# Kernel tuning notes

Hardware: AMD Instinct MI355X
Metric: run time of the kernel (lower is better)

## Reference

```python
import jax, jax.numpy as jnp
import numpy as np

# Static config (matches init_kwargs)
VOCAB, EMBED, HIDDEN = 32000, 256, 512
SLOTS, MEM_DIM, HEADS, TOPK = 1024, 64, 4, 8
B, T = 16, 128
# beta_read/beta_write are learned scalars but the torch forward detaches them
# via .item(); treat as constants (|beta| + 1e-6 with beta init ~1.0).
BETA_R = 1.0 + 1e-6
BETA_W = 1.0 + 1e-6
EPS = 1e-8


def setup_inputs() -> dict:
    key = jax.random.key(0)
    ks = jax.random.split(key, 16)
    s = 0.02
    HD = HEADS * MEM_DIM
    return {
        "input_seq": jax.random.randint(ks[0], (B, T), 0, VOCAB),
        "E": jax.random.normal(ks[1], (VOCAB, EMBED), jnp.float32) * s,
        "W_ih": jax.random.normal(ks[2], (4 * HIDDEN, EMBED + MEM_DIM), jnp.float32) * s,
        "W_hh": jax.random.normal(ks[3], (4 * HIDDEN, HIDDEN), jnp.float32) * s,
        "b_ih": jnp.zeros((4 * HIDDEN,), jnp.float32),
        "b_hh": jnp.zeros((4 * HIDDEN,), jnp.float32),
        "W_out": jax.random.normal(ks[4], (HIDDEN, VOCAB), jnp.float32) * s,
        "b_out": jnp.zeros((VOCAB,), jnp.float32),
        "W_rk": jax.random.normal(ks[5], (HIDDEN, HD), jnp.float32) * s,
        "b_rk": jnp.zeros((HD,), jnp.float32),
        "W_wk": jax.random.normal(ks[6], (HIDDEN, HD), jnp.float32) * s,
        "b_wk": jnp.zeros((HD,), jnp.float32),
        "W_wv": jax.random.normal(ks[7], (HIDDEN, HD), jnp.float32) * s,
        "b_wv": jnp.zeros((HD,), jnp.float32),
        "W_er": jax.random.normal(ks[8], (HIDDEN, HD), jnp.float32) * s,
        "b_er": jnp.zeros((HD,), jnp.float32),
    }


def _address(memory, keys, beta):
    # memory: [B,S,D], keys: [B,H,D] -> sparse (top-k) content weights [B,H,S]
    mem_n = memory / (jnp.linalg.norm(memory, axis=-1, keepdims=True) + EPS)
    key_n = keys / (jnp.linalg.norm(keys, axis=-1, keepdims=True) + EPS)
    scores = beta * jnp.einsum("bhd,bsd->bhs", key_n, mem_n)
    vals, idx = jax.lax.top_k(scores, TOPK)           # [B,H,K]
    sm = jax.nn.softmax(vals, axis=-1)                # softmax over top-k only
    w = jnp.zeros_like(scores)
    b_ix = jnp.arange(scores.shape[0])[:, None, None]
    h_ix = jnp.arange(HEADS)[None, :, None]
    return w.at[b_ix, h_ix, idx].set(sm)              # [B,H,S]


def reference(input_seq, E, W_ih, W_hh, b_ih, b_hh, W_out, b_out,
              W_rk, b_rk, W_wk, b_wk, W_wv, b_wv, W_er, b_er):
    Bq = input_seq.shape[0]
    memory0 = jnp.full((Bq, SLOTS, MEM_DIM), 1e-6, jnp.float32)
    h0 = jnp.zeros((Bq, HIDDEN), jnp.float32)
    c0 = jnp.zeros((Bq, HIDDEN), jnp.float32)
    r0 = jnp.zeros((Bq, MEM_DIM), jnp.float32)

    def step(carry, x_t):
        memory, h, c, read_vec = carry
        emb = E[x_t]                                          # [B,embed]
        inp = jnp.concatenate([emb, read_vec], axis=-1)
        gates = inp @ W_ih.T + b_ih + h @ W_hh.T + b_hh       # [B,4H]
        i, f, g, o = jnp.split(gates, 4, axis=-1)             # torch LSTM order
        c = jax.nn.sigmoid(f) * c + jax.nn.sigmoid(i) * jnp.tanh(g)
        h = jax.nn.sigmoid(o) * jnp.tanh(c)
        logits = h @ W_out + b_out                            # [B,V]
        rk = (h @ W_rk + b_rk).reshape(Bq, HEADS, MEM_DIM)
        wk = (h @ W_wk + b_wk).reshape(Bq, HEADS, MEM_DIM)
        wv = (h @ W_wv + b_wv).reshape(Bq, HEADS, MEM_DIM)
        er = jax.nn.sigmoid(h @ W_er + b_er).reshape(Bq, HEADS, MEM_DIM)
        # content-addressed top-k read
        rw = _address(memory, rk, BETA_R)                     # [B,H,S]
        read_vec = jnp.einsum("bhs,bsd->bhd", rw, memory).mean(axis=1)
        # erase + add write
        ww = _address(memory, wk, BETA_W)                     # [B,H,S]
        keep = jnp.prod(1.0 - ww[..., None] * er[:, :, None, :], axis=1)
        add = jnp.einsum("bhs,bhd->bsd", ww, wv)
        memory = memory * keep + add
        return (memory, h, c, read_vec), logits

    _, logits_seq = jax.lax.scan(step, (memory0, h0, c0, r0), input_seq.T)
    return jnp.transpose(logits_seq, (1, 0, 2))               # [B,T,V]
```

## Files before the change

kernel.cpp:

```cpp
#include <hip/hip_runtime.h>
#include <hip/hip_bf16.h>
#include <stdint.h>

typedef unsigned int uint;
typedef unsigned long long u64;

#define T_STEPS 128
#define BQ 16
#define HID 512
#define XROW 580
#define WROW 516
#define NSLOT 1024
#define MD 64
#define VOCAB 32000
#define NWG 128
#define BETA 1.000001f
#define EPSN 1e-8f

#define OFF_NRM 8704
#define OFF_WS  8832
#define OFF_SCR 12960
#define SMEM_F  22496

#define AL4(dst, p) asm volatile("global_load_dwordx4 %0, %1, off sc0 sc1" : "=v"(dst) : "v"(p))
#define ALF(dst, p) asm volatile("global_load_dword %0, %1, off sc0 sc1" : "=v"(dst) : "v"(p))
#define AWAIT() do { asm volatile("s_waitcnt vmcnt(0)" ::: "memory"); __builtin_amdgcn_sched_barrier(0); } while(0)

__device__ __forceinline__ float sigm(float x){ return 1.f/(1.f+expf(-x)); }
__device__ __forceinline__ void astoref(float* p, float v){
  __hip_atomic_store(p, v, __ATOMIC_RELAXED, __HIP_MEMORY_SCOPE_AGENT);
}
__device__ __forceinline__ void astoreu64(u64* p, u64 v){
  __hip_atomic_store(p, v, __ATOMIC_RELAXED, __HIP_MEMORY_SCOPE_AGENT);
}
__device__ __forceinline__ u64 aloadu64(const u64* p){
  return __hip_atomic_load((u64*)p, __ATOMIC_RELAXED, __HIP_MEMORY_SCOPE_AGENT);
}

__device__ __forceinline__ u64 packsc(float v, int slot){
  uint u = __float_as_uint(v);
  u = (u & 0x80000000u) ? ~u : (u | 0x80000000u);
  return ((u64)u << 10) | (u64)(1023 - slot);
}
__device__ __forceinline__ float unpackval(u64 p){
  uint u = (uint)(p >> 10);
  uint bits = (u & 0x80000000u) ? (u & 0x7fffffffu) : ~u;
  return __uint_as_float(bits);
}
__device__ __forceinline__ int unpackslot(u64 p){ return 1023 - (int)(p & 1023u); }

__device__ __forceinline__ void gbar(uint* arrv, uint& ls){
  asm volatile("s_waitcnt vmcnt(0)" ::: "memory");
  __syncthreads();
  ls++;
  if (threadIdx.x == 0)
    __hip_atomic_store(arrv + (size_t)blockIdx.x*32, ls, __ATOMIC_RELAXED, __HIP_MEMORY_SCOPE_AGENT);
  if (threadIdx.x < NWG){
    while (__hip_atomic_load(arrv + (size_t)threadIdx.x*32, __ATOMIC_RELAXED, __HIP_MEMORY_SCOPE_AGENT) < ls)
      __builtin_amdgcn_s_sleep(1);
  }
  __syncthreads();
}

__global__ __launch_bounds__(256) void prep_emb(const float* __restrict__ E,
                                                const int* __restrict__ seq,
                                                float* __restrict__ EMB){
  int m = blockIdx.x;
  int t = m >> 4, b = m & 15;
  int x = seq[b*T_STEPS + t];
  EMB[(size_t)m*256 + threadIdx.x] = E[(size_t)x*256 + threadIdx.x];
}

__global__ __launch_bounds__(256) void gemm_emb(const float* __restrict__ A,
                                                const float* __restrict__ W_ih,
                                                const float* __restrict__ b_ih,
                                                const float* __restrict__ b_hh,
                                                float* __restrict__ C){
  __shared__ __align__(16) float As[16*68];
  __shared__ __align__(16) float Bs[16*68];
  int mt = blockIdx.x & 31, nt = blockIdx.x >> 5;
  int m0 = mt*64, n0 = nt*64;
  int tx = threadIdx.x & 15, ty = threadIdx.x >> 4;
  float acc[4][4] = {};
  for (int k0 = 0; k0 < 256; k0 += 16){
    int mm = threadIdx.x >> 2, kq = (threadIdx.x & 3)*4;
    float4 a = *(const float4*)(A + (size_t)(m0+mm)*256 + k0 + kq);
    As[(kq+0)*68+mm]=a.x; As[(kq+1)*68+mm]=a.y; As[(kq+2)*68+mm]=a.z; As[(kq+3)*68+mm]=a.w;
    int pp = n0 + mm;
    int r = (pp & 3)*512 + (pp >> 2);
    float4 bv = *(const float4*)(W_ih + (size_t)r*320 + k0 + kq);
    Bs[(kq+0)*68+mm]=bv.x; Bs[(kq+1)*68+mm]=bv.y; Bs[(kq+2)*68+mm]=bv.z; Bs[(kq+3)*68+mm]=bv.w;
    __syncthreads();
    #pragma unroll
    for (int kk = 0; kk < 16; ++kk){
      float4 av = *(const float4*)(As + kk*68 + ty*4);
      float4 bb = *(const float4*)(Bs + kk*68 + tx*4);
      float aa[4] = {av.x,av.y,av.z,av.w};
      float bv2[4] = {bb.x,bb.y,bb.z,bb.w};
      #pragma unroll
      for (int i = 0; i < 4; ++i)
        #pragma unroll
        for (int j = 0; j < 4; ++j)
          acc[i][j] = fmaf(aa[i], bv2[j], acc[i][j]);
    }
    __syncthreads();
  }
  #pragma unroll
  for (int i = 0; i < 4; ++i){
    int m = m0 + ty*4 + i;
    #pragma unroll
    for (int j = 0; j < 4; ++j){
      int pp = n0 + tx*4 + j;
      int r = (pp & 3)*512 + (pp >> 2);
      C[(size_t)m*2048 + pp] = acc[i][j] + b_ih[r] + b_hh[r];
    }
  }
}

__global__ __launch_bounds__(256, 1) void recurrent_kernel(
    const float* __restrict__ W_hh, const float* __restrict__ W_ih,
    const float* __restrict__ W_rk, const float* __restrict__ b_rk,
    const float* __restrict__ W_wk, const float* __restrict__ b_wk,
    const float* __restrict__ W_wv, const float* __restrict__ b_wv,
    const float* __restrict__ W_er, const float* __restrict__ b_er,
    const float* __restrict__ G_emb, float* __restrict__ H_all,
    float* __restrict__ mem_g, float* __restrict__ projbuf,
    float* __restrict__ rv_g, u64* __restrict__ cand,
    u64* __restrict__ wlist, uint* __restrict__ arrv)
{
  __shared__ __align__(16) float smem[SMEM_F];
  const int tid = threadIdx.x;
  const int wg  = blockIdx.x;
  uint ls = 0;
  float c_reg = 0.f;

  const int p1_b = tid >> 4, p1_col = tid & 15;
  const int pcol = wg*16 + p1_col;
  const int rrow = (pcol & 3)*512 + (pcol >> 2);

  const int msel = wg >> 5;
  const int col0 = (wg & 31)*8;
  const float* Wm = (msel==0)? W_rk : (msel==1)? W_wk : (msel==2)? W_wv : W_er;
  const float* bm = (msel==0)? b_rk : (msel==1)? b_wk : (msel==2)? b_wv : b_er;
  {
    float* Ws = smem + OFF_WS;
    for (int i = tid; i < 8*HID; i += 256){
      int k = i >> 3, j = i & 7;
      Ws[j*WROW + k] = Wm[(size_t)k*256 + col0 + j];
    }
  }
  const int bb3 = wg >> 3, rg = wg & 7, s0 = rg*128;
  float* mslice_g = mem_g + ((size_t)bb3*NSLOT + s0)*MD;

  #pragma clang loop unroll(disable)
  for (int t = 0; t < T_STEPS; ++t){
    {
      float* xs = smem + OFF_SCR;
      float* gl = smem + OFF_SCR + 9280;
      if (t > 0){
        const float4* hsrc = (const float4*)(H_all + (size_t)(t-1)*BQ*HID);
        for (int i = tid; i < BQ*HID/4; i += 256){
          int b = i >> 7, q = i & 127;
          *(float4*)(xs + b*XROW + q*4) = hsrc[i];
        }
        {
          int b = tid >> 4, dq = tid & 15;
          float4 rvv;
          AL4(rvv, (const float4*)(rv_g + (size_t)b*MD) + dq);
          AWAIT();
          *(float4*)(xs + b*XROW + 512 + dq*4) = rvv;
        }
      } else {
        for (int i = tid; i < BQ*XROW; i += 256) xs[i] = 0.f;
      }
      __syncthreads();
      {
        float a0 = G_emb[(size_t)(t*BQ + p1_b)*2048 + pcol];
        float a1 = 0.f, a2 = 0.f, a3 = 0.f;
        const float4* wh = (const float4*)(W_hh + (size_t)rrow*HID);
        const float4* xv = (const float4*)(xs + p1_b*XROW);
        #pragma unroll 2
        for (int k = 0; k < 128; k += 4){
          float4 w, x;
          w=wh[k+0]; x=xv[k+0]; a0=fmaf(w.x,x.x,a0); a0=fmaf(w.y,x.y,a0); a0=fmaf(w.z,x.z,a0); a0=fmaf(w.w,x.w,a0);
          w=wh[k+1]; x=xv[k+1]; a1=fmaf(w.x,x.x,a1); a1=fmaf(w.y,x.y,a1); a1=fmaf(w.z,x.z,a1); a1=fmaf(w.w,x.w,a1);
          w=wh[k+2]; x=xv[k+2]; a2=fmaf(w.x,x.x,a2); a2=fmaf(w.y,x.y,a2); a2=fmaf(w.z,x.z,a2); a2=fmaf(w.w,x.w,a2);
          w=wh[k+3]; x=xv[k+3]; a3=fmaf(w.x,x.x,a3); a3=fmaf(w.y,x.y,a3); a3=fmaf(w.z,x.z,a3); a3=fmaf(w.w,x.w,a3);
        }
        const float4* wi = (const float4*)(W_ih + (size_t)rrow*320 + 256);
        const float4* xr = (const float4*)(xs + p1_b*XROW + 512);
        #pragma unroll
        for (int k = 0; k < 16; k += 4){
          float4 w, x;
          w=wi[k+0]; x=xr[k+0]; a0=fmaf(w.x,x.x,a0); a0=fmaf(w.y,x.y,a0); a0=fmaf(w.z,x.z,a0); a0=fmaf(w.w,x.w,a0);
          w=wi[k+1]; x=xr[k+1]; a1=fmaf(w.x,x.x,a1); a1=fmaf(w.y,x.y,a1); a1=fmaf(w.z,x.z,a1); a1=fmaf(w.w,x.w,a1);
          w=wi[k+2]; x=xr[k+2]; a2=fmaf(w.x,x.x,a2); a2=fmaf(w.y,x.y,a2); a2=fmaf(w.z,x.z,a2); a2=fmaf(w.w,x.w,a2);
          w=wi[k+3]; x=xr[k+3]; a3=fmaf(w.x,x.x,a3); a3=fmaf(w.y,x.y,a3); a3=fmaf(w.z,x.z,a3); a3=fmaf(w.w,x.w,a3);
        }
        gl[p1_b*16 + p1_col] = (a0+a1)+(a2+a3);
      }
      __syncthreads();
      if (p1_col < 4){
        float gi = gl[p1_b*16 + p1_col*4 + 0];
        float gf = gl[p1_b*16 + p1_col*4 + 1];
        float gg = gl[p1_b*16 + p1_col*4 + 2];
        float go = gl[p1_b*16 + p1_col*4 + 3];
        c_reg = sigm(gf)*c_reg + sigm(gi)*tanhf(gg);
        float h = sigm(go)*tanhf(c_reg);
        astoref(H_all + (size_t)(t*BQ + p1_b)*HID + wg*4 + p1_col, h);
      }
    }
    gbar(arrv, ls);

    {
      float* hs = smem + OFF_SCR;
      float* Ws = smem + OFF_WS;
      const float4* hsrc = (const float4*)(H_all + (size_t)t*BQ*HID);
      for (int i = tid; i < BQ*HID/4; i += 256){
        int b = i >> 7, q = i & 127;
        *(float4*)(hs + b*WROW + q*4) = hsrc[i];
      }
      __syncthreads();
      int b = tid >> 4, o2 = (tid & 15) >> 1, half = tid & 1;
      const float4* wp = (const float4*)(Ws + o2*WROW + half*256);
      const float4* xp = (const float4*)(hs + b*WROW + half*256);
      float a0 = 0.f, a1 = 0.f;
      #pragma unroll 4
      for (int k = 0; k < 64; k += 2){
        float4 w = wp[k], x = xp[k];
        a0=fmaf(w.x,x.x,a0); a0=fmaf(w.y,x.y,a0); a0=fmaf(w.z,x.z,a0); a0=fmaf(w.w,x.w,a0);
        w = wp[k+1]; x = xp[k+1];
        a1=fmaf(w.x,x.x,a1); a1=fmaf(w.y,x.y,a1); a1=fmaf(w.z,x.z,a1); a1=fmaf(w.w,x.w,a1);
      }
      float acc = a0 + a1;
      float other = __shfl_xor(acc, 1);
      if (half == 0){
        float v = acc + other + bm[col0 + o2];
        if (msel == 3) v = sigm(v);
        astoref(projbuf + (size_t)(t&1)*BQ*1024 + (size_t)b*1024 + msel*256 + col0 + o2, v);
      }
    }
    gbar(arrv, ls);

    {
      float* mem_s  = smem;
      float* nrm_s  = smem + OFF_NRM;
      float* scr    = smem + OFF_SCR;
      u64*   wl_s   = (u64*)scr;
      float* key_s  = scr + 64;
      float* er_s   = scr + 576;
      float* wv_s   = scr + 832;
      float* knrm_s = scr + 1088;
      float* sc_s   = scr + 1096;
      const int par = t & 1, parp = par ^ 1;
      const float* projb = projbuf + (size_t)par*BQ*1024 + (size_t)bb3*1024;
      const float* projp = projbuf + (size_t)parp*BQ*1024 + (size_t)bb3*1024;

      if (tid >= 128){
        int i = tid - 128;
        float4 kv;
        AL4(kv, (const float4*)projb + i);
        AWAIT();
        *(float4*)(key_s + i*4) = kv;
      } else if (t == 0){
        for (int i = tid; i < 128*MD; i += 128){
          int row = i >> 6, d = i & 63;
          mem_s[row*68 + d] = 1e-6f;
          astoref(mslice_g + i, 1e-6f);
        }
      } else {
        if (tid < 32)
          wl_s[tid] = aloadu64(wlist + (size_t)bb3*32 + tid);
        if (tid < 64){
          float4 v; AL4(v, (const float4*)(projp + 512) + tid); AWAIT();
          *(float4*)(wv_s + tid*4) = v;
        } else {
          int i = tid - 64;
          float4 v; AL4(v, (const float4*)(projp + 768) + i); AWAIT();
          *(float4*)(er_s + i*4) = v;
        }
      }
      __syncthreads();
      if (t > 0 && tid < 64){
        const int d = tid;
        #pragma unroll 1
        for (int e = 0; e < 32; ++e){
          u64 w64 = wl_s[e];
          int sl = (int)(w64 & 0xffffffffu);
          if (sl >= s0 && sl < s0+128){
            float w = __uint_as_float((uint)(w64 >> 32));
            int h = e >> 3;
            mem_s[(sl-s0)*68 + d] *= (1.f - w*er_s[h*64 + d]);
          }
        }
        #pragma unroll 1
        for (int e = 0; e < 32; ++e){
          u64 w64 = wl_s[e];
          int sl = (int)(w64 & 0xffffffffu);
          if (sl >= s0 && sl < s0+128){
            float w = __uint_as_float((uint)(w64 >> 32));
            int h = e >> 3;
            mem_s[(sl-s0)*68 + d] += w*wv_s[h*64 + d];
          }
        }
        #pragma unroll 1
        for (int e = 0; e < 32; ++e){
          u64 w64 = wl_s[e];
          int sl = (int)(w64 & 0xffffffffu);
          if (sl >= s0 && sl < s0+128)
            astoref(mslice_g + (sl-s0)*MD + d, mem_s[(sl-s0)*68 + d]);
        }
      }
      __syncthreads();
      {
        int s = tid >> 1, half = tid & 1;
        const float4* mp = (const float4*)(mem_s + s*68 + half*32);
        float sum = 0.f;
        #pragma unroll
        for (int q = 0; q < 8; ++q){
          float4 v = mp[q];
          sum = fmaf(v.x,v.x,sum); sum = fmaf(v.y,v.y,sum);
          sum = fmaf(v.z,v.z,sum); sum = fmaf(v.w,v.w,sum);
        }
        sum += __shfl_xor(sum, 1);
        if (half == 0) nrm_s[s] = sqrtf(sum) + EPSN;
      }
      if (tid < 8){
        const float4* kp = (const float4*)(key_s + tid*MD);
        float sum = 0.f;
        #pragma unroll
        for (int q = 0; q < 16; ++q){
          float4 v = kp[q];
          sum = fmaf(v.x,v.x,sum); sum = fmaf(v.y,v.y,sum);
          sum = fmaf(v.z,v.z,sum); sum = fmaf(v.w,v.w,sum);
        }
        knrm_s[tid] = sqrtf(sum) + EPSN;
      }
      __syncthreads();
      {
        int s = tid >> 1, kh = tid & 1;
        const float4* mp = (const float4*)(mem_s + s*68);
        float rnm = 1.f / nrm_s[s];
        float acc4[4] = {0.f,0.f,0.f,0.f};
        #pragma unroll
        for (int q = 0; q < 16; ++q){
          float4 m = mp[q];
          #pragma unroll
          for (int kk = 0; kk < 4; ++kk){
            float4 k4 = *(const float4*)(key_s + (kh*4+kk)*MD + q*4);
            acc4[kk] = fmaf(m.x,k4.x,acc4[kk]); acc4[kk] = fmaf(m.y,k4.y,acc4[kk]);
            acc4[kk] = fmaf(m.z,k4.z,acc4[kk]); acc4[kk] = fmaf(m.w,k4.w,acc4[kk]);
          }
        }
        #pragma unroll
        for (int kk = 0; kk < 4; ++kk){
          int key = kh*4 + kk;
          sc_s[key*128 + s] = BETA * acc4[kk] * rnm / knrm_s[key];
        }
      }
      __syncthreads();
      {
        int wid = tid >> 6, lane = tid & 63;
        #pragma unroll
        for (int kk = 0; kk < 2; ++kk){
          int key = wid*2 + kk;
          u64 p0 = packsc(sc_s[key*128 + lane],      s0 + lane);
          u64 p1 = packsc(sc_s[key*128 + 64 + lane], s0 + 64 + lane);
          #pragma unroll
          for (int r = 0; r < 8; ++r){
            u64 m = p0 > p1 ? p0 : p1;
            #pragma unroll
            for (int o = 32; o; o >>= 1){ u64 q = __shfl_xor(m, o); if (q > m) m = q; }
            if (p0 == m) p0 = 0; else if (p1 == m) p1 = 0;
            if (lane == 0) astoreu64(cand + (((size_t)bb3*8 + key)*8 + rg)*8 + r, m);
          }
        }
      }
    }
    gbar(arrv, ls);

    if (wg < BQ){
      const int bb = wg;
      float* rvp = smem + OFF_SCR;
      int wid = tid >> 6, lane = tid & 63;
      #pragma unroll
      for (int kk = 0; kk < 2; ++kk){
        int key = wid*2 + kk;
        u64 pv = aloadu64(cand + (((size_t)bb*8 + key)*8 + (lane >> 3))*8 + (lane & 7));
        u64 sel = 0;
        #pragma unroll
        for (int r = 0; r < 8; ++r){
          u64 m = pv;
          #pragma unroll
          for (int o = 32; o; o >>= 1){ u64 q = __shfl_xor(m, o); if (q > m) m = q; }
          if (pv == m) pv = 0;
          if (lane == r) sel = m;
        }
        float val = unpackval(sel);
        int slot = unpackslot(sel);
        float vmax = __shfl(val, 0);
        float e = (lane < 8) ? expf(val - vmax) : 0.f;
        float ssum = e;
        #pragma unroll
        for (int o = 32; o; o >>= 1) ssum += __shfl_xor(ssum, o);
        float w = e / ssum;
        if (key < 4){
          int sls[8];
          #pragma unroll
          for (int i = 0; i < 8; ++i) sls[i] = __shfl(slot, i);
          float mv[8];
          #pragma unroll
          for (int i = 0; i < 8; ++i)
            ALF(mv[i], mem_g + ((size_t)bb*NSLOT + sls[i])*MD + lane);
          AWAIT();
          float acc = 0.f;
          #pragma unroll
          for (int i = 0; i < 8; ++i) acc = fmaf(__shfl(w, i), mv[i], acc);
          rvp[key*64 + lane] = acc;
        } else if (lane < 8){
          astoreu64(wlist + (size_t)bb*32 + (key-4)*8 + lane,
                    ((u64)__float_as_uint(w) << 32) | (u64)(uint)slot);
        }
      }
      __syncthreads();
      if (tid < 64){
        float m = 0.25f*(rvp[tid] + rvp[64+tid] + rvp[128+tid] + rvp[192+tid]);
        astoref(rv_g + (size_t)bb*MD + tid, m);
      }
    }
    gbar(arrv, ls);
  }
}

__global__ __launch_bounds__(256) void gemm_out(const float* __restrict__ A,
                                                const float* __restrict__ Bmat,
                                                const float* __restrict__ bias,
                                                float* __restrict__ C){
  __shared__ __align__(16) float As[16*132];
  __shared__ __align__(16) float Bs[16*64];
  int mt = blockIdx.x & 15, nt = blockIdx.x >> 4;
  int m0 = mt*128, n0 = nt*64;
  int tx = threadIdx.x & 15, ty = threadIdx.x >> 4;
  float acc[8][4] = {};
  for (int k0 = 0; k0 < 512; k0 += 16){
    int mm = threadIdx.x >> 1, kq = (threadIdx.x & 1)*8;
    float4 a0 = *(const float4*)(A + (size_t)(m0+mm)*512 + k0 + kq);
    float4 a1 = *(const float4*)(A + (size_t)(m0+mm)*512 + k0 + kq + 4);
    As[(kq+0)*132+mm]=a0.x; As[(kq+1)*132+mm]=a0.y; As[(kq+2)*132+mm]=a0.z; As[(kq+3)*132+mm]=a0.w;
    As[(kq+4)*132+mm]=a1.x; As[(kq+5)*132+mm]=a1.y; As[(kq+6)*132+mm]=a1.z; As[(kq+7)*132+mm]=a1.w;
    int kk2 = threadIdx.x >> 4, nq = (threadIdx.x & 15)*4;
    *(float4*)(Bs + kk2*64 + nq) = *(const float4*)(Bmat + (size_t)(k0+kk2)*VOCAB + n0 + nq);
    __syncthreads();
    #pragma unroll
    for (int kk = 0; kk < 16; ++kk){
      float4 x0 = *(const float4*)(As + kk*132 + ty*8);
      float4 x1 = *(const float4*)(As + kk*132 + ty*8 + 4);
      float4 bv = *(const float4*)(Bs + kk*64 + tx*4);
      float aa[8] = {x0.x,x0.y,x0.z,x0.w,x1.x,x1.y,x1.z,x1.w};
      float bb[4] = {bv.x,bv.y,bv.z,bv.w};
      #pragma unroll
      for (int i = 0; i < 8; ++i)
        #pragma unroll
        for (int j = 0; j < 4; ++j)
          acc[i][j] = fmaf(aa[i], bb[j], acc[i][j]);
    }
    __syncthreads();
  }
  #pragma unroll
  for (int i = 0; i < 8; ++i){
    int m = m0 + ty*8 + i;
    int bq = m & 15, tt = m >> 4;
    float* crow = C + ((size_t)bq*T_STEPS + tt)*VOCAB + n0 + tx*4;
    #pragma unroll
    for (int j = 0; j < 4; ++j) crow[j] = acc[i][j] + bias[n0 + tx*4 + j];
  }
}

extern "C" void kernel_launch(void* const* d_in, const int* in_sizes, int n_in,
                              void* d_out, int out_size, void* d_ws, size_t ws_size,
                              hipStream_t stream){
  const int*   seq   = (const int*)d_in[0];
  const float* E     = (const float*)d_in[1];
  const float* W_ih  = (const float*)d_in[2];
  const float* W_hh  = (const float*)d_in[3];
  const float* b_ih  = (const float*)d_in[4];
  const float* b_hh  = (const float*)d_in[5];
  const float* W_out = (const float*)d_in[6];
  const float* b_out = (const float*)d_in[7];
  const float* W_rk  = (const float*)d_in[8];
  const float* b_rk  = (const float*)d_in[9];
  const float* W_wk  = (const float*)d_in[10];
  const float* b_wk  = (const float*)d_in[11];
  const float* W_wv  = (const float*)d_in[12];
  const float* b_wv  = (const float*)d_in[13];
  const float* W_er  = (const float*)d_in[14];
  const float* b_er  = (const float*)d_in[15];
  float* out = (float*)d_out;
  (void)in_sizes; (void)n_in; (void)out_size; (void)ws_size;

  char* ws = (char*)d_ws;
  size_t off = 0;
  auto alloc = [&](size_t bytes) -> void* {
    off = (off + 255) & ~(size_t)255;
    void* p = ws + off;
    off += bytes;
    return p;
  };
  float* EMB     = (float*)alloc((size_t)2048*256*4);
  float* G_emb   = (float*)alloc((size_t)2048*2048*4);
  float* H_all   = (float*)alloc((size_t)2048*512*4);
  float* memb    = (float*)alloc((size_t)16*1024*64*4);
  float* projbuf = (float*)alloc((size_t)2*16*1024*4);
  float* rv_g    = (float*)alloc((size_t)16*64*4);
  u64*   cand    = (u64*)alloc((size_t)16*8*8*8*8);
  u64*   wlist   = (u64*)alloc((size_t)16*32*8);
  uint*  arrv    = (uint*)alloc((size_t)NWG*32*4);

  hipMemsetAsync(arrv, 0, (size_t)NWG*32*4, stream);
  prep_emb<<<2048, 256, 0, stream>>>(E, seq, EMB);
  gemm_emb<<<1024, 256, 0, stream>>>(EMB, W_ih, b_ih, b_hh, G_emb);
  recurrent_kernel<<<NWG, 256, 0, stream>>>(W_hh, W_ih, W_rk, b_rk, W_wk, b_wk,
                                            W_wv, b_wv, W_er, b_er,
                                            G_emb, H_all, memb, projbuf, rv_g,
                                            cand, wlist, arrv);
  gemm_out<<<16*500, 256, 0, stream>>>(H_all, W_out, b_out, out);
}
```

Measured before the change: 7.330 ms.

## Overlap W_hh matvec with memory update and use a hierarchical grid barrier

```diff
diff --git a/kernel.cpp b/kernel.cpp
--- a/kernel.cpp
+++ b/kernel.cpp
@@ -8,8 +8,6 @@
 #define T_STEPS 128
 #define BQ 16
 #define HID 512
-#define XROW 580
-#define WROW 516
 #define NSLOT 1024
 #define MD 64
 #define VOCAB 32000
@@ -17,10 +15,19 @@
 #define BETA 1.000001f
 #define EPSN 1e-8f
 
-#define OFF_NRM 8704
-#define OFF_WS  8832
-#define OFF_SCR 12960
-#define SMEM_F  22496
+#define L_MEM  0
+#define L_NRM  8704
+#define L_WS   8832
+#define L_HS   12960
+#define L_KEY  21216
+#define L_KNRM 21728
+#define L_SC   21736
+#define L_WV   22760
+#define L_ER   23016
+#define L_WL   23272
+#define L_GL   23336
+#define L_RV   23592
+#define L_TOT  24616
 
 #define AL4(dst, p) asm volatile("global_load_dwordx4 %0, %1, off sc0 sc1" : "=v"(dst) : "v"(p))
 #define ALF(dst, p) asm volatile("global_load_dword %0, %1, off sc0 sc1" : "=v"(dst) : "v"(p))
@@ -35,6 +42,9 @@
 }
 __device__ __forceinline__ u64 aloadu64(const u64* p){
   return __hip_atomic_load((u64*)p, __ATOMIC_RELAXED, __HIP_MEMORY_SCOPE_AGENT);
+}
+__device__ __forceinline__ uint aloadu32(const uint* p){
+  return __hip_atomic_load((uint*)p, __ATOMIC_RELAXED, __HIP_MEMORY_SCOPE_AGENT);
 }
 
 __device__ __forceinline__ u64 packsc(float v, int slot){
@@ -49,17 +59,29 @@
 }
 __device__ __forceinline__ int unpackslot(u64 p){ return 1023 - (int)(p & 1023u); }
 
-__device__ __forceinline__ void gbar(uint* arrv, uint& ls){
+__device__ __forceinline__ void b_arrive(uint* arrv, uint gen){
   asm volatile("s_waitcnt vmcnt(0)" ::: "memory");
   __syncthreads();
-  ls++;
   if (threadIdx.x == 0)
-    __hip_atomic_store(arrv + (size_t)blockIdx.x*32, ls, __ATOMIC_RELAXED, __HIP_MEMORY_SCOPE_AGENT);
-  if (threadIdx.x < NWG){
-    while (__hip_atomic_load(arrv + (size_t)threadIdx.x*32, __ATOMIC_RELAXED, __HIP_MEMORY_SCOPE_AGENT) < ls)
-      __builtin_amdgcn_s_sleep(1);
-  }
-  __syncthreads();
+    __hip_atomic_store(arrv + (size_t)blockIdx.x*32, gen, __ATOMIC_RELAXED, __HIP_MEMORY_SCOPE_AGENT);
+}
+__device__ __forceinline__ void b_wait(uint* arrv, uint gen){
+  if (blockIdx.x == 0){
+    if (threadIdx.x < NWG){
+      while (aloadu32(arrv + (size_t)threadIdx.x*32) < gen)
+        __builtin_amdgcn_s_sleep(1);
+    }
+    __syncthreads();
+    if (threadIdx.x < 16)
+      __hip_atomic_store(arrv + (size_t)(NWG + threadIdx.x)*32, gen, __ATOMIC_RELAXED, __HIP_MEMORY_SCOPE_AGENT);
+    __syncthreads();
+  } else {
+    if (threadIdx.x == 0){
+      while (aloadu32(arrv + (size_t)(NWG + (blockIdx.x & 15))*32) < gen)
+        __builtin_amdgcn_s_sleep(1);
+    }
+    __syncthreads();
+  }
 }
 
 __global__ __launch_bounds__(256) void prep_emb(const float* __restrict__ E,
@@ -128,102 +150,70 @@
     float* __restrict__ rv_g, u64* __restrict__ cand,
     u64* __restrict__ wlist, uint* __restrict__ arrv)
 {
-  __shared__ __align__(16) float smem[SMEM_F];
+  __shared__ __align__(16) float smem[L_TOT];
+  float* mem_s  = smem + L_MEM;
+  float* nrm_s  = smem + L_NRM;
+  float* Ws     = smem + L_WS;
+  float* hs     = smem + L_HS;
+  float* key_s  = smem + L_KEY;
+  float* knrm_s = smem + L_KNRM;
+  float* sc_s   = smem + L_SC;
+  float* wv_s   = smem + L_WV;
+  float* er_s   = smem + L_ER;
+  u64*   wl_s   = (u64*)(smem + L_WL);
+  float* gl     = smem + L_GL;
+  float* rv_st  = smem + L_RV;
+
   const int tid = threadIdx.x;
   const int wg  = blockIdx.x;
-  uint ls = 0;
   float c_reg = 0.f;
 
   const int p1_b = tid >> 4, p1_col = tid & 15;
   const int pcol = wg*16 + p1_col;
   const int rrow = (pcol & 3)*512 + (pcol >> 2);
-
   const int msel = wg >> 5;
   const int col0 = (wg & 31)*8;
-  const float* Wm = (msel==0)? W_rk : (msel==1)? W_wk : (msel==2)? W_wv : W_er;
-  const float* bm = (msel==0)? b_rk : (msel==1)? b_wk : (msel==2)? b_wv : b_er;
-  {
-    float* Ws = smem + OFF_WS;
-    for (int i = tid; i < 8*HID; i += 256){
-      int k = i >> 3, j = i & 7;
-      Ws[j*WROW + k] = Wm[(size_t)k*256 + col0 + j];
-    }
-  }
+  const float* Wm  = (msel==0)? W_rk : (msel==1)? W_wk : (msel==2)? W_wv : W_er;
+  const float* bmp = (msel==0)? b_rk : (msel==1)? b_wk : (msel==2)? b_wv : b_er;
   const int bb3 = wg >> 3, rg = wg & 7, s0 = rg*128;
   float* mslice_g = mem_g + ((size_t)bb3*NSLOT + s0)*MD;
 
+  for (int i = tid; i < 8*HID; i += 256){
+    int k = i >> 3, j = i & 7;
+    Ws[j*516 + k] = Wm[(size_t)k*256 + col0 + j];
+  }
+  for (int i = tid; i < 128*MD; i += 256){
+    mem_s[(i >> 6)*68 + (i & 63)] = 1e-6f;
+    astoref(mslice_g + i, 1e-6f);
+  }
+  gl[p1_b*16 + p1_col] = G_emb[(size_t)p1_b*2048 + pcol];
+  __syncthreads();
+  if (p1_col < 4){
+    float gi = gl[p1_b*16 + p1_col*4 + 0];
+    float gf = gl[p1_b*16 + p1_col*4 + 1];
+    float gg = gl[p1_b*16 + p1_col*4 + 2];
+    float go = gl[p1_b*16 + p1_col*4 + 3];
+    c_reg = sigm(gf)*c_reg + sigm(gi)*tanhf(gg);
+    float h = sigm(go)*tanhf(c_reg);
+    astoref(H_all + (size_t)p1_b*HID + wg*4 + p1_col, h);
+  }
+  b_arrive(arrv, 1);
+
   #pragma clang loop unroll(disable)
-  for (int t = 0; t < T_STEPS; ++t){
+  for (int t = 0; t < T_STEPS-1; ++t){
+    const uint g0 = (uint)(4*t);
+    b_wait(arrv, g0 + 1);
+
     {
-      float* xs = smem + OFF_SCR;
-      float* gl = smem + OFF_SCR + 9280;
-      if (t > 0){
-        const float4* hsrc = (const float4*)(H_all + (size_t)(t-1)*BQ*HID);
-        for (int i = tid; i < BQ*HID/4; i += 256){
-          int b = i >> 7, q = i & 127;
-          *(float4*)(xs + b*XROW + q*4) = hsrc[i];
-        }
-        {
-          int b = tid >> 4, dq = tid & 15;
-          float4 rvv;
-          AL4(rvv, (const float4*)(rv_g + (size_t)b*MD) + dq);
-          AWAIT();
-          *(float4*)(xs + b*XROW + 512 + dq*4) = rvv;
-        }
-      } else {
-        for (int i = tid; i < BQ*XROW; i += 256) xs[i] = 0.f;
-      }
-      __syncthreads();
-      {
-        float a0 = G_emb[(size_t)(t*BQ + p1_b)*2048 + pcol];
-        float a1 = 0.f, a2 = 0.f, a3 = 0.f;
-        const float4* wh = (const float4*)(W_hh + (size_t)rrow*HID);
-        const float4* xv = (const float4*)(xs + p1_b*XROW);
-        #pragma unroll 2
-        for (int k = 0; k < 128; k += 4){
-          float4 w, x;
-          w=wh[k+0]; x=xv[k+0]; a0=fmaf(w.x,x.x,a0); a0=fmaf(w.y,x.y,a0); a0=fmaf(w.z,x.z,a0); a0=fmaf(w.w,x.w,a0);
-          w=wh[k+1]; x=xv[k+1]; a1=fmaf(w.x,x.x,a1); a1=fmaf(w.y,x.y,a1); a1=fmaf(w.z,x.z,a1); a1=fmaf(w.w,x.w,a1);
-          w=wh[k+2]; x=xv[k+2]; a2=fmaf(w.x,x.x,a2); a2=fmaf(w.y,x.y,a2); a2=fmaf(w.z,x.z,a2); a2=fmaf(w.w,x.w,a2);
-          w=wh[k+3]; x=xv[k+3]; a3=fmaf(w.x,x.x,a3); a3=fmaf(w.y,x.y,a3); a3=fmaf(w.z,x.z,a3); a3=fmaf(w.w,x.w,a3);
-        }
-        const float4* wi = (const float4*)(W_ih + (size_t)rrow*320 + 256);
-        const float4* xr = (const float4*)(xs + p1_b*XROW + 512);
-        #pragma unroll
-        for (int k = 0; k < 16; k += 4){
-          float4 w, x;
-          w=wi[k+0]; x=xr[k+0]; a0=fmaf(w.x,x.x,a0); a0=fmaf(w.y,x.y,a0); a0=fmaf(w.z,x.z,a0); a0=fmaf(w.w,x.w,a0);
-          w=wi[k+1]; x=xr[k+1]; a1=fmaf(w.x,x.x,a1); a1=fmaf(w.y,x.y,a1); a1=fmaf(w.z,x.z,a1); a1=fmaf(w.w,x.w,a1);
-          w=wi[k+2]; x=xr[k+2]; a2=fmaf(w.x,x.x,a2); a2=fmaf(w.y,x.y,a2); a2=fmaf(w.z,x.z,a2); a2=fmaf(w.w,x.w,a2);
-          w=wi[k+3]; x=xr[k+3]; a3=fmaf(w.x,x.x,a3); a3=fmaf(w.y,x.y,a3); a3=fmaf(w.z,x.z,a3); a3=fmaf(w.w,x.w,a3);
-        }
-        gl[p1_b*16 + p1_col] = (a0+a1)+(a2+a3);
-      }
-      __syncthreads();
-      if (p1_col < 4){
-        float gi = gl[p1_b*16 + p1_col*4 + 0];
-        float gf = gl[p1_b*16 + p1_col*4 + 1];
-        float gg = gl[p1_b*16 + p1_col*4 + 2];
-        float go = gl[p1_b*16 + p1_col*4 + 3];
-        c_reg = sigm(gf)*c_reg + sigm(gi)*tanhf(gg);
-        float h = sigm(go)*tanhf(c_reg);
-        astoref(H_all + (size_t)(t*BQ + p1_b)*HID + wg*4 + p1_col, h);
-      }
-    }
-    gbar(arrv, ls);
-
-    {
-      float* hs = smem + OFF_SCR;
-      float* Ws = smem + OFF_WS;
       const float4* hsrc = (const float4*)(H_all + (size_t)t*BQ*HID);
       for (int i = tid; i < BQ*HID/4; i += 256){
         int b = i >> 7, q = i & 127;
-        *(float4*)(hs + b*WROW + q*4) = hsrc[i];
+        *(float4*)(hs + b*516 + q*4) = hsrc[i];
       }
       __syncthreads();
       int b = tid >> 4, o2 = (tid & 15) >> 1, half = tid & 1;
-      const float4* wp = (const float4*)(Ws + o2*WROW + half*256);
-      const float4* xp = (const float4*)(hs + b*WROW + half*256);
+      const float4* wp = (const float4*)(Ws + o2*516 + half*256);
+      const float4* xp = (const float4*)(hs + b*516 + half*256);
       float a0 = 0.f, a1 = 0.f;
       #pragma unroll 4
       for (int k = 0; k < 64; k += 2){
@@ -235,46 +225,24 @@
       float acc = a0 + a1;
       float other = __shfl_xor(acc, 1);
       if (half == 0){
-        float v = acc + other + bm[col0 + o2];
+        float v = acc + other + bmp[col0 + o2];
         if (msel == 3) v = sigm(v);
         astoref(projbuf + (size_t)(t&1)*BQ*1024 + (size_t)b*1024 + msel*256 + col0 + o2, v);
       }
     }
-    gbar(arrv, ls);
-
+    b_arrive(arrv, g0 + 2);
+
+    float gp;
     {
-      float* mem_s  = smem;
-      float* nrm_s  = smem + OFF_NRM;
-      float* scr    = smem + OFF_SCR;
-      u64*   wl_s   = (u64*)scr;
-      float* key_s  = scr + 64;
-      float* er_s   = scr + 576;
-      float* wv_s   = scr + 832;
-      float* knrm_s = scr + 1088;
-      float* sc_s   = scr + 1096;
-      const int par = t & 1, parp = par ^ 1;
-      const float* projb = projbuf + (size_t)par*BQ*1024 + (size_t)bb3*1024;
-      const float* projp = projbuf + (size_t)parp*BQ*1024 + (size_t)bb3*1024;
-
-      if (tid >= 128){
-        int i = tid - 128;
-        float4 kv;
-        AL4(kv, (const float4*)projb + i);
-        AWAIT();
-        *(float4*)(key_s + i*4) = kv;
-      } else if (t == 0){
-        for (int i = tid; i < 128*MD; i += 128){
-          int row = i >> 6, d = i & 63;
-          mem_s[row*68 + d] = 1e-6f;
-          astoref(mslice_g + i, 1e-6f);
-        }
-      } else {
+      const int parp = (t & 1) ^ 1;
+      if (t > 0){
+        const float* projp = projbuf + (size_t)parp*BQ*1024 + (size_t)bb3*1024;
         if (tid < 32)
           wl_s[tid] = aloadu64(wlist + (size_t)bb3*32 + tid);
         if (tid < 64){
           float4 v; AL4(v, (const float4*)(projp + 512) + tid); AWAIT();
           *(float4*)(wv_s + tid*4) = v;
-        } else {
+        } else if (tid < 128){
           int i = tid - 64;
           float4 v; AL4(v, (const float4*)(projp + 768) + i); AWAIT();
           *(float4*)(er_s + i*4) = v;
@@ -289,8 +257,7 @@
           int sl = (int)(w64 & 0xffffffffu);
           if (sl >= s0 && sl < s0+128){
             float w = __uint_as_float((uint)(w64 >> 32));
-            int h = e >> 3;
-            mem_s[(sl-s0)*68 + d] *= (1.f - w*er_s[h*64 + d]);
+            mem_s[(sl-s0)*68 + d] *= (1.f - w*er_s[(e >> 3)*64 + d]);
           }
         }
         #pragma unroll 1
@@ -299,8 +266,7 @@
           int sl = (int)(w64 & 0xffffffffu);
           if (sl >= s0 && sl < s0+128){
             float w = __uint_as_float((uint)(w64 >> 32));
-            int h = e >> 3;
-            mem_s[(sl-s0)*68 + d] += w*wv_s[h*64 + d];
+            mem_s[(sl-s0)*68 + d] += w*wv_s[(e >> 3)*64 + d];
           }
         }
         #pragma unroll 1
@@ -325,6 +291,31 @@
         sum += __shfl_xor(sum, 1);
         if (half == 0) nrm_s[s] = sqrtf(sum) + EPSN;
       }
+      {
+        float a0 = G_emb[(size_t)((t+1)*BQ + p1_b)*2048 + pcol];
+        float a1 = 0.f, a2 = 0.f, a3 = 0.f;
+        const float4* wh = (const float4*)(W_hh + (size_t)rrow*HID);
+        const float4* xv = (const float4*)(hs + p1_b*516);
+        #pragma unroll 2
+        for (int k = 0; k < 128; k += 4){
+          float4 w, x;
+          w=wh[k+0]; x=xv[k+0]; a0=fmaf(w.x,x.x,a0); a0=fmaf(w.y,x.y,a0); a0=fmaf(w.z,x.z,a0); a0=fmaf(w.w,x.w,a0);
+          w=wh[k+1]; x=xv[k+1]; a1=fmaf(w.x,x.x,a1); a1=fmaf(w.y,x.y,a1); a1=fmaf(w.z,x.z,a1); a1=fmaf(w.w,x.w,a1);
+          w=wh[k+2]; x=xv[k+2]; a2=fmaf(w.x,x.x,a2); a2=fmaf(w.y,x.y,a2); a2=fmaf(w.z,x.z,a2); a2=fmaf(w.w,x.w,a2);
+          w=wh[k+3]; x=xv[k+3]; a3=fmaf(w.x,x.x,a3); a3=fmaf(w.y,x.y,a3); a3=fmaf(w.w,x.w,a3); a3=fmaf(w.z,x.z,a3);
+        }
+        gp = (a0+a1)+(a2+a3);
+      }
+    }
+    b_wait(arrv, g0 + 2);
+
+    {
+      const float* projb = projbuf + (size_t)(t&1)*BQ*1024 + (size_t)bb3*1024;
+      if (tid < 128){
+        float4 kv; AL4(kv, (const float4*)projb + tid); AWAIT();
+        *(float4*)(key_s + tid*4) = kv;
+      }
+      __syncthreads();
       if (tid < 8){
         const float4* kp = (const float4*)(key_s + tid*MD);
         float sum = 0.f;
@@ -377,11 +368,11 @@
         }
       }
     }
-    gbar(arrv, ls);
+    b_arrive(arrv, g0 + 3);
+    b_wait(arrv, g0 + 3);
 
     if (wg < BQ){
       const int bb = wg;
-      float* rvp = smem + OFF_SCR;
       int wid = tid >> 6, lane = tid & 63;
       #pragma unroll
       for (int kk = 0; kk < 2; ++kk){
@@ -416,7 +407,7 @@
           float acc = 0.f;
           #pragma unroll
           for (int i = 0; i < 8; ++i) acc = fmaf(__shfl(w, i), mv[i], acc);
-          rvp[key*64 + lane] = acc;
+          rv_st[key*64 + lane] = acc;
         } else if (lane < 8){
           astoreu64(wlist + (size_t)bb*32 + (key-4)*8 + lane,
                     ((u64)__float_as_uint(w) << 32) | (u64)(uint)slot);
@@ -424,11 +415,40 @@
       }
       __syncthreads();
       if (tid < 64){
-        float m = 0.25f*(rvp[tid] + rvp[64+tid] + rvp[128+tid] + rvp[192+tid]);
+        float m = 0.25f*(rv_st[tid] + rv_st[64+tid] + rv_st[128+tid] + rv_st[192+tid]);
         astoref(rv_g + (size_t)bb*MD + tid, m);
       }
     }
-    gbar(arrv, ls);
+    b_arrive(arrv, g0 + 4);
+    b_wait(arrv, g0 + 4);
+
+    {
+      float4 rvv; AL4(rvv, (const float4*)rv_g + tid); AWAIT();
+      *(float4*)(rv_st + tid*4) = rvv;
+      __syncthreads();
+      float a0 = gp, a1 = 0.f;
+      const float4* wi = (const float4*)(W_ih + (size_t)rrow*320 + 256);
+      const float4* xr = (const float4*)(rv_st + p1_b*64);
+      #pragma unroll
+      for (int k = 0; k < 16; k += 2){
+        float4 w = wi[k], x = xr[k];
+        a0=fmaf(w.x,x.x,a0); a0=fmaf(w.y,x.y,a0); a0=fmaf(w.z,x.z,a0); a0=fmaf(w.w,x.w,a0);
+        w = wi[k+1]; x = xr[k+1];
+        a1=fmaf(w.x,x.x,a1); a1=fmaf(w.y,x.y,a1); a1=fmaf(w.z,x.z,a1); a1=fmaf(w.w,x.w,a1);
+      }
+      gl[p1_b*16 + p1_col] = a0 + a1;
+      __syncthreads();
+      if (p1_col < 4){
+        float gi = gl[p1_b*16 + p1_col*4 + 0];
+        float gf = gl[p1_b*16 + p1_col*4 + 1];
+        float gg = gl[p1_b*16 + p1_col*4 + 2];
+        float go = gl[p1_b*16 + p1_col*4 + 3];
+        c_reg = sigm(gf)*c_reg + sigm(gi)*tanhf(gg);
+        float h = sigm(go)*tanhf(c_reg);
+        astoref(H_all + (size_t)((t+1)*BQ + p1_b)*HID + wg*4 + p1_col, h);
+      }
+    }
+    b_arrive(arrv, g0 + 5);
   }
 }
 
@@ -514,9 +534,9 @@
   float* rv_g    = (float*)alloc((size_t)16*64*4);
   u64*   cand    = (u64*)alloc((size_t)16*8*8*8*8);
   u64*   wlist   = (u64*)alloc((size_t)16*32*8);
-  uint*  arrv    = (uint*)alloc((size_t)NWG*32*4);
-
-  hipMemsetAsync(arrv, 0, (size_t)NWG*32*4, stream);
+  uint*  arrv    = (uint*)alloc((size_t)(NWG+16)*32*4);
+
+  hipMemsetAsync(arrv, 0, (size_t)(NWG+16)*32*4, stream);
   prep_emb<<<2048, 256, 0, stream>>>(E, seq, EMB);
   gemm_emb<<<1024, 256, 0, stream>>>(EMB, W_ih, b_ih, b_hh, G_emb);
   recurrent_kernel<<<NWG, 256, 0, stream>>>(W_hh, W_ih, W_rk, b_rk, W_wk, b_wk,
```

New measurement: 7.368 ms. No clear change (+0.5%).
